# Optimization experiments

Measured on AMD Instinct MI355X. Metric: run time of the kernel, lower is better.

The kernel has to match this reference:

```python
import jax, jax.numpy as jnp
import numpy as np
from math import factorial, sqrt

# ---------------- irreps / instruction metadata ----------------
LS = [0, 1, 2]
MULS_IN = [128, 64, 32]      # node_irreps = 128x0e + 64x1o + 32x2e
HC = 32                      # hidden_channels -> mixed_irreps = 32x0e+32x1o+32x2e
# feasible 'uuw' instructions (parity-even outputs 0e,1e,2e)
INSTR = [(0,0,0),(1,1,0),(2,2,0),(1,1,1),(2,2,1),(0,2,2),(2,0,2),(1,1,2),(2,2,2)]
PATHS = {0: 3, 1: 2, 2: 4}

# ---------------- real Clebsch-Gordan coefficients ----------------
def _cg(l1, l2, l3):
    """Complex CG <l1 m1 l2 m2 | l3 m3>, shape [2l1+1,2l2+1,2l3+1]."""
    f = lambda n: float(factorial(n))
    C = np.zeros((2*l1+1, 2*l2+1, 2*l3+1))
    for m1 in range(-l1, l1+1):
        for m2 in range(-l2, l2+1):
            m3 = m1 + m2
            if abs(m3) > l3:
                continue
            pre = sqrt((2*l3+1) * f(l1+l2-l3)*f(l1-l2+l3)*f(-l1+l2+l3)/f(l1+l2+l3+1))
            pre *= sqrt(f(l3+m3)*f(l3-m3)*f(l1-m1)*f(l1+m1)*f(l2-m2)*f(l2+m2))
            s = 0.0
            for k in range(0, l1+l2-l3+1):
                d = [k, l1+l2-l3-k, l1-m1-k, l2+m2-k, l3-l2+m1+k, l3-l1-m2+k]
                if any(x < 0 for x in d):
                    continue
                s += (-1)**k / np.prod([f(x) for x in d])
            C[m1+l1, m2+l2, m3+l3] = pre * s
    return C

def _u_real(l):
    """Complex->real spherical harmonic change of basis (rows: real m)."""
    U = np.zeros((2*l+1, 2*l+1), dtype=complex)
    U[l, l] = 1.0
    for m in range(1, l+1):
        U[l+m, l+m] = (-1)**m / sqrt(2)
        U[l+m, l-m] = 1.0 / sqrt(2)
        U[l-m, l+m] = -1j*(-1)**m / sqrt(2)
        U[l-m, l-m] = 1j / sqrt(2)
    return U

def _real_cg(l1, l2, l3):
    """Real CG tensor, Frobenius norm 1 (like e3nn wigner_3j)."""
    C = _cg(l1, l2, l3).astype(complex)
    R = np.einsum('am,bn,co,mno->abc', _u_real(l1), _u_real(l2), np.conj(_u_real(l3)), C)
    Rr = R.real if np.abs(R.real).max() >= np.abs(R.imag).max() else R.imag
    return (Rr / np.linalg.norm(Rr)).astype(np.float32)

RCG = {k: _real_cg(*k) for k in set(INSTR)}
# Cartesian rank-2 change of basis: 3x3 tensor = 0e + 1e + 2e; orthonormal basis matrices
QB = {l: _real_cg(1, 1, l) * sqrt(2*l + 1) for l in LS}   # [3,3,2l+1]

def _split(x, muls):
    outs, off = [], 0
    for mul, l in zip(muls, LS):
        d = mul * (2*l + 1)
        outs.append(x[:, off:off+d].reshape(-1, mul, 2*l + 1))
        off += d
    return outs


def setup_inputs() -> dict:
    key = jax.random.key(0)
    ks = jax.random.split(key, 14)
    N, B = 50000, 500
    dim_sph = sum(m*(2*l+1) for m, l in zip(MULS_IN, LS))   # 480
    return {
        'x_scalar':    jax.random.normal(ks[0], (N, 128), jnp.float32),
        'x_spherical': jax.random.normal(ks[1], (N, dim_sph), jnp.float32),
        'batch':       jnp.sort(jax.random.randint(ks[2], (N,), 0, B)),
        'num_graphs':  B,
        'W0': jax.random.normal(ks[3], (128, HC), jnp.float32),
        'W1': jax.random.normal(ks[4], (64,  HC), jnp.float32),
        'W2': jax.random.normal(ks[5], (32,  HC), jnp.float32),
        'A1': jax.random.normal(ks[6], (128, 64), jnp.float32) / sqrt(128),
        'b1': jnp.zeros((64,), jnp.float32),
        'A2': jax.random.normal(ks[7], (64, 9*HC), jnp.float32) / sqrt(64),
        'b2': jnp.zeros((9*HC,), jnp.float32),
        'p0': jax.random.normal(ks[8], (3,), jnp.float32),
        'p1': jax.random.normal(ks[9], (2,), jnp.float32),
        'p2': jax.random.normal(ks[10], (4,), jnp.float32),
    }


def reference(x_scalar, x_spherical, batch, num_graphs,
              W0, W1, W2, A1, b1, A2, b2, p0, p1, p2):
    # ---- SelfMixTP: per-l linear mix to HC channels + per-irrep-block RMS norm ----
    xs_in = _split(x_spherical, MULS_IN)
    xs = []
    for x, W in zip(xs_in, [W0, W1, W2]):
        y = jnp.einsum('num,uv->nvm', x, W) / sqrt(W.shape[0])
        rms = jnp.sqrt(jnp.mean(y*y, axis=(1, 2), keepdims=True) + 1e-5)
        xs.append(y / rms)                       # [N, HC, 2l+1]
    # ---- per-node TP weights ----
    h = jax.nn.silu(x_scalar @ A1 + b1)
    tp_w = h @ A2 + b2                           # [N, 9*HC]
    # ---- weighted uuw CG tensor product ----
    outs = {0: [], 1: [], 2: []}
    off = 0
    for (la, lb, lo) in INSTR:
        w = tp_w[:, off:off+HC]; off += HC       # [N, HC]
        R = jnp.asarray(RCG[(la, lb, lo)])       # [2la+1, 2lb+1, 2lo+1]
        alpha = sqrt(2*lo + 1.0) / sqrt(PATHS[lo] * HC)
        xa = xs[la] * w[:, :, None]              # fold per-node weights into one factor
        y = jnp.einsum('nua,abc->nubc', xa, R)
        y = jnp.einsum('nubc,nub->nc', y, xs[lb]) * alpha
        outs[lo].append(y)
    # ---- post linear: collapse paths per l (sph_irreps -> rtp_irreps) ----
    sph = []
    for l, p in zip(LS, [p0, p1, p2]):
        stk = jnp.stack(outs[l], axis=1)         # [N, P_l, 2l+1]
        sph.append(jnp.einsum('npm,p->nm', stk, p) / sqrt(stk.shape[1]))
    # ---- Sph2Cart: spherical (0e+1e+2e) -> cartesian 3x3 ----
    x_cart = sum(jnp.einsum('nm,ijm->nij', sph[l], jnp.asarray(QB[l])) for l in LS)
    # ---- scatter-sum over graphs ----
    g = jax.ops.segment_sum(x_cart, batch, num_segments=num_graphs)  # [B,3,3]
    # ---- roll each cartesian axis by 1 (yzx -> xyz reordering) ----
    return jnp.roll(jnp.roll(g, 1, axis=1), 1, axis=2)
```

## Files before the change

### kernel.cpp

```cpp
#include <hip/hip_runtime.h>
#include <math.h>


#define N_CG_FLOATS 438

typedef short s16x8 __attribute__((ext_vector_type(8)));
typedef short s16x4 __attribute__((ext_vector_type(4)));
typedef float f32x4 __attribute__((ext_vector_type(4)));

#define PK_BYTE_OFF 2048
#define PK_A1 0
#define PK_W0 8192
#define PK_A2 12288
#define PK_W1 30720
#define PK_W2 32768
#define PK_TOTAL 33792

__device__ __forceinline__ short f2bf(float f) {
  union { float f; unsigned u; } x; x.f = f;
  unsigned r = (x.u + 0x7FFFu + ((x.u >> 16) & 1u)) >> 16;
  return (short)r;
}
__device__ __forceinline__ float bf2f(unsigned short s) {
  union { unsigned u; float f; } x; x.u = ((unsigned)s) << 16;
  return x.f;
}


__device__ __forceinline__ double dfact(int n) {
  double r = 1.0;
  for (int i = 2; i <= n; ++i) r *= (double)i;
  return r;
}

__device__ __forceinline__ void u_elem(int l, int i, int j, double& re, double& im) {
  re = 0.0; im = 0.0;
  const int mr = i - l, mc = j - l;
  const double is2 = 0.70710678118654752440;
  if (mr == 0) { if (mc == 0) re = 1.0; }
  else if (mr > 0) {
    if (mc == mr) re = ((mr & 1) ? -1.0 : 1.0) * is2;
    else if (mc == -mr) re = is2;
  } else {
    int m = -mr;
    if (mc == m) im = -(((m & 1) ? -1.0 : 1.0)) * is2;
    else if (mc == -m) im = is2;
  }
}

__global__ void setup_cg_par(float* __restrict__ ws) {
  const int LAs[12] = {0, 1, 2, 1, 2, 0, 2, 1, 2, 1, 1, 1};
  const int LBs[12] = {0, 1, 2, 1, 2, 2, 0, 1, 2, 1, 1, 1};
  const int LOs[12] = {0, 0, 0, 1, 1, 2, 2, 2, 2, 0, 1, 2};
  const int OFF[12] = {0, 1, 10, 35, 62, 137, 162, 187, 232, 357, 366, 393};

  const int blk = blockIdx.x;
  const int l1 = LAs[blk], l2 = LBs[blk], l3 = LOs[blk];
  const double scale = (blk >= 9) ? sqrt(2.0 * l3 + 1.0) : 1.0;
  const int n1 = 2 * l1 + 1, n2 = 2 * l2 + 1, n3 = 2 * l3 + 1;
  const int nel = n1 * n2 * n3;
  const int t = threadIdx.x;

  __shared__ double Cs[125];
  __shared__ double Rre[125], Rim[125];
  __shared__ double s_inv;
  __shared__ int s_useRe;

  if (t < nel) {
    const int i3 = t % n3, i2 = (t / n3) % n2, i1 = t / (n3 * n2);
    const int m1 = i1 - l1, m2 = i2 - l2, m3 = i3 - l3;
    double val = 0.0;
    if (m1 + m2 == m3) {
      double pre = sqrt((2.0 * l3 + 1.0) * dfact(l1 + l2 - l3) * dfact(l1 - l2 + l3) *
                        dfact(-l1 + l2 + l3) / dfact(l1 + l2 + l3 + 1));
      pre *= sqrt(dfact(l3 + m3) * dfact(l3 - m3) * dfact(l1 - m1) * dfact(l1 + m1) *
                  dfact(l2 - m2) * dfact(l2 + m2));
      double s = 0.0;
      for (int k = 0; k <= l1 + l2 - l3; ++k) {
        int d1 = l1 + l2 - l3 - k, d2 = l1 - m1 - k, d3 = l2 + m2 - k;
        int d4 = l3 - l2 + m1 + k, d5 = l3 - l1 - m2 + k;
        if (d1 < 0 || d2 < 0 || d3 < 0 || d4 < 0 || d5 < 0) continue;
        double prod = dfact(k) * dfact(d1) * dfact(d2) * dfact(d3) * dfact(d4) * dfact(d5);
        s += ((k & 1) ? -1.0 : 1.0) / prod;
      }
      val = pre * s;
    }
    Cs[t] = val;
  }
  __syncthreads();

  if (t < nel) {
    const int c = t % n3, bb = (t / n3) % n2, a = t / (n3 * n2);
    double sr_ = 0.0, si_ = 0.0;
    for (int m = 0; m < n1; ++m) {
      double u1r, u1i;
      u_elem(l1, a, m, u1r, u1i);
      if (u1r == 0.0 && u1i == 0.0) continue;
      for (int nn = 0; nn < n2; ++nn) {
        double u2r, u2i;
        u_elem(l2, bb, nn, u2r, u2i);
        double t12r = u1r * u2r - u1i * u2i;
        double t12i = u1r * u2i + u1i * u2r;
        if (t12r == 0.0 && t12i == 0.0) continue;
        for (int o = 0; o < n3; ++o) {
          double cgv = Cs[(m * n2 + nn) * n3 + o];
          if (cgv == 0.0) continue;
          double u3r, u3i;
          u_elem(l3, c, o, u3r, u3i);
          sr_ += (t12r * u3r + t12i * u3i) * cgv;
          si_ += (t12i * u3r - t12r * u3i) * cgv;
        }
      }
    }
    Rre[t] = sr_;
    Rim[t] = si_;
  }
  __syncthreads();

  if (t == 0) {
    double maxRe = 0.0, maxIm = 0.0;
    for (int e = 0; e < nel; ++e) {
      maxRe = fmax(maxRe, fabs(Rre[e]));
      maxIm = fmax(maxIm, fabs(Rim[e]));
    }
    int useRe = (maxRe >= maxIm) ? 1 : 0;
    double nrm = 0.0;
    for (int e = 0; e < nel; ++e) {
      double vv = useRe ? Rre[e] : Rim[e];
      nrm += vv * vv;
    }
    s_useRe = useRe;
    s_inv = scale / sqrt(nrm);
  }
  __syncthreads();

  if (t < nel) {
    double vv = s_useRe ? Rre[t] : Rim[t];
    ws[OFF[blk] + t] = (float)(vv * s_inv);
  }
}

__global__ void pack_weights(const float* __restrict__ A1, const float* __restrict__ W0,
                             const float* __restrict__ A2, const float* __restrict__ W1,
                             const float* __restrict__ W2, float* __restrict__ ws) {
  unsigned short* pk = (unsigned short*)((char*)ws + PK_BYTE_OFF);
  int e = blockIdx.x * 256 + threadIdx.x;
  if (e >= PK_TOTAL) return;
  const float* src;
  int Ncols, off;
  float scale;
  if (e < PK_W0)      { src = A1; Ncols = 64;  off = PK_A1; scale = 1.f; }
  else if (e < PK_A2) { src = W0; Ncols = 32;  off = PK_W0; scale = 0.08838834764831845f; }
  else if (e < PK_W1) { src = A2; Ncols = 288; off = PK_A2; scale = 1.f; }
  else if (e < PK_W2) { src = W1; Ncols = 32;  off = PK_W1; scale = 0.125f; }
  else                { src = W2; Ncols = 32;  off = PK_W2; scale = 0.17677669529663687f; }
  int local = e - off;
  int frag = local >> 9;
  int l = (local >> 3) & 63;
  int j = local & 7;
  int ntn = Ncols >> 4;
  int kt = frag / ntn, nt = frag - kt * ntn;
  int k = kt * 32 + 8 * (l >> 4) + j;
  int c = nt * 16 + (l & 15);
  pk[e] = (unsigned short)f2bf(src[k * Ncols + c] * scale);
}


__device__ __forceinline__ s16x8 cvt8(const float* __restrict__ g) {
  float4 a = *(const float4*)g;
  float4 b = *(const float4*)(g + 4);
  s16x8 r;
  r[0] = f2bf(a.x); r[1] = f2bf(a.y); r[2] = f2bf(a.z); r[3] = f2bf(a.w);
  r[4] = f2bf(b.x); r[5] = f2bf(b.y); r[6] = f2bf(b.z); r[7] = f2bf(b.w);
  return r;
}

__device__ __forceinline__ void sw_wr8(char* sm, int base, int strideB, int r, int c0, s16x8 v) {
  int byte = base + r * strideB + c0 * 2;
  byte ^= (r & 7) << 4;
  *(s16x8*)(sm + byte) = v;
}
__device__ __forceinline__ s16x8 sw_lda16(const char* sm, int base, int strideB, int k0,
                                          int lane) {
  int r = lane & 15;
  int byte = base + r * strideB + (k0 + 8 * (lane >> 4)) * 2;
  byte ^= (r & 7) << 4;
  return *(const s16x8*)(sm + byte);
}

template <int LA, int LB, int LO>
__device__ __forceinline__ void tp_accum(const float* __restrict__ R, float w,
                                         const float* xa, const float* xb, float* sph) {
  constexpr int NA = 2 * LA + 1, NB = 2 * LB + 1, NC = 2 * LO + 1;
#pragma unroll
  for (int a = 0; a < NA; ++a) {
#pragma unroll
    for (int b = 0; b < NB; ++b) {
      float xab = xa[a] * xb[b] * w;
#pragma unroll
      for (int c = 0; c < NC; ++c) sph[c] = fmaf(xab, R[(a * NB + b) * NC + c], sph[c]);
    }
  }
}

#define F_XS 0
#define F_SP 4096
#define F_H  8192
#define F_P1 10240
#define F_P2 16384
#define F_TW 10240
#define F_YA 21504
#define F_SMEM 30720

__global__ __launch_bounds__(256) void mega_fused(
    const float* __restrict__ xs_g, const float* __restrict__ sp_g,
    const int* __restrict__ batch, const float* __restrict__ b1,
    const float* __restrict__ b2, const float* __restrict__ p0,
    const float* __restrict__ p1, const float* __restrict__ p2,
    const float* __restrict__ ws, float* __restrict__ out, int N) {
  __shared__ char sm[F_SMEM];
  const unsigned short* pk = (const unsigned short*)((const char*)ws + PK_BYTE_OFF);
  const float* cg = ws;

  const int t = threadIdx.x;
  const int b0 = blockIdx.x * 16;
  const int lane = t & 63;
  const int wid = t >> 6;

  {
    int n = t >> 4, c0 = (t & 15) * 8;
    long nn = min((long)(b0 + n), (long)N - 1);
    sw_wr8(sm, F_XS, 256, n, c0, cvt8(xs_g + nn * 128 + c0));
    sw_wr8(sm, F_SP, 256, n, c0, cvt8(sp_g + nn * 480 + c0));
  }
  {
    int n = t >> 4, uc = t & 15;
    long nn = min((long)(b0 + n), (long)N - 1);
    const float* g = sp_g + nn * 480 + 128 + uc * 12;
    float4 a0 = *(const float4*)(g), a1 = *(const float4*)(g + 4), a2 = *(const float4*)(g + 8);
    float fl[12] = {a0.x, a0.y, a0.z, a0.w, a1.x, a1.y, a1.z, a1.w, a2.x, a2.y, a2.z, a2.w};
#pragma unroll
    for (int m = 0; m < 3; ++m) {
      s16x4 e;
#pragma unroll
      for (int j = 0; j < 4; ++j) e[j] = f2bf(fl[j * 3 + m]);
      int byte = F_P1 + m * 2048 + n * 128 + uc * 8;
      byte ^= (n & 7) << 4;
      *(s16x4*)(sm + byte) = e;
    }
  }
  if (t < 128) {
    int n = t >> 3, uc = t & 7;
    long nn = min((long)(b0 + n), (long)N - 1);
    const float* g = sp_g + nn * 480 + 320 + uc * 20;
    float4 a0 = *(const float4*)(g), a1 = *(const float4*)(g + 4), a2 = *(const float4*)(g + 8),
           a3 = *(const float4*)(g + 12), a4 = *(const float4*)(g + 16);
    float fl[20] = {a0.x, a0.y, a0.z, a0.w, a1.x, a1.y, a1.z, a1.w, a2.x, a2.y,
                    a2.z, a2.w, a3.x, a3.y, a3.z, a3.w, a4.x, a4.y, a4.z, a4.w};
#pragma unroll
    for (int m = 0; m < 5; ++m) {
      s16x4 e;
#pragma unroll
      for (int j = 0; j < 4; ++j) e[j] = f2bf(fl[j * 5 + m]);
      int byte = F_P2 + m * 1024 + n * 64 + uc * 8;
      byte ^= (n & 7) << 4;
      *(s16x4*)(sm + byte) = e;
    }
  }
  __syncthreads();

  {
    f32x4 acc = {0.f, 0.f, 0.f, 0.f};
#pragma unroll
    for (int kt = 0; kt < 4; ++kt) {
      s16x8 a = sw_lda16(sm, F_XS, 256, kt * 32, lane);
      s16x8 b = *(const s16x8*)(pk + PK_A1 + (((kt << 2) + wid) * 64 + lane) * 8);
      acc = __builtin_amdgcn_mfma_f32_16x16x32_bf16(a, b, acc, 0, 0, 0);
    }
    const int col = wid * 16 + (lane & 15);
    const int r0 = (lane >> 4) * 4;
    const float bb = b1[col];
#pragma unroll
    for (int q = 0; q < 4; ++q) {
      float hv = acc[q] + bb;
      hv = hv / (1.f + __expf(-hv));
      int r = r0 + q;
      int byte = F_H + r * 128 + col * 2;
      byte ^= (r & 7) << 4;
      *(short*)(sm + byte) = f2bf(hv);
    }
  }

  const int r0 = (lane >> 4) * 4;
  if (wid < 2) {
    f32x4 acc = {0.f, 0.f, 0.f, 0.f};
#pragma unroll
    for (int kt = 0; kt < 4; ++kt) {
      s16x8 a = sw_lda16(sm, F_SP, 256, kt * 32, lane);
      s16x8 b = *(const s16x8*)(pk + PK_W0 + (((kt << 1) + wid) * 64 + lane) * 8);
      acc = __builtin_amdgcn_mfma_f32_16x16x32_bf16(a, b, acc, 0, 0, 0);
    }
    const int col = wid * 16 + (lane & 15);
#pragma unroll
    for (int q = 0; q < 4; ++q)
      *(short*)(sm + F_YA + (r0 + q) * 576 + col * 2) = f2bf(acc[q]);
  }
  for (int tl = wid; tl < 6; tl += 4) {
    const int m = tl >> 1, nt = tl & 1;
    f32x4 acc = {0.f, 0.f, 0.f, 0.f};
#pragma unroll
    for (int kt = 0; kt < 2; ++kt) {
      s16x8 a = sw_lda16(sm, F_P1 + m * 2048, 128, kt * 32, lane);
      s16x8 b = *(const s16x8*)(pk + PK_W1 + (((kt << 1) + nt) * 64 + lane) * 8);
      acc = __builtin_amdgcn_mfma_f32_16x16x32_bf16(a, b, acc, 0, 0, 0);
    }
    const int col = 32 + m * 32 + nt * 16 + (lane & 15);
#pragma unroll
    for (int q = 0; q < 4; ++q)
      *(short*)(sm + F_YA + (r0 + q) * 576 + col * 2) = f2bf(acc[q]);
  }
  for (int tl = wid; tl < 10; tl += 4) {
    const int m = tl >> 1, nt = tl & 1;
    f32x4 acc = {0.f, 0.f, 0.f, 0.f};
    {
      s16x8 a = sw_lda16(sm, F_P2 + m * 1024, 64, 0, lane);
      s16x8 b = *(const s16x8*)(pk + PK_W2 + (nt * 64 + lane) * 8);
      acc = __builtin_amdgcn_mfma_f32_16x16x32_bf16(a, b, acc, 0, 0, 0);
    }
    const int col = 128 + m * 32 + nt * 16 + (lane & 15);
#pragma unroll
    for (int q = 0; q < 4; ++q)
      *(short*)(sm + F_YA + (r0 + q) * 576 + col * 2) = f2bf(acc[q]);
  }
  __syncthreads();

  for (int tl = wid; tl < 18; tl += 4) {
    f32x4 acc = {0.f, 0.f, 0.f, 0.f};
#pragma unroll
    for (int kt = 0; kt < 2; ++kt) {
      s16x8 a = sw_lda16(sm, F_H, 128, kt * 32, lane);
      s16x8 b = *(const s16x8*)(pk + PK_A2 + ((kt * 18 + tl) * 64 + lane) * 8);
      acc = __builtin_amdgcn_mfma_f32_16x16x32_bf16(a, b, acc, 0, 0, 0);
    }
    const int col = tl * 16 + (lane & 15);
    const float bb = b2[col];
#pragma unroll
    for (int q = 0; q < 4; ++q)
      *(short*)(sm + F_TW + (r0 + q) * 576 + col * 2) = f2bf(acc[q] + bb);
  }
  __syncthreads();

  const int v = t & 31;
  const int sl = t >> 5;
  const float invs32 = 0.17677669529663687f;
  const float k0c = invs32 / 3.0f;
  const float k1c = 1.7320508075688772f * invs32 / 2.0f;
  const float k2c = 2.23606797749979f * invs32 / 4.0f;
  const float c0 = k0c * p0[0], c1 = k0c * p0[1], c2 = k0c * p0[2];
  const float c3 = k1c * p1[0], c4 = k1c * p1[1];
  const float c5 = k2c * p2[0], c6 = k2c * p2[1], c7 = k2c * p2[2], c8 = k2c * p2[3];
  const float* qb0 = cg + 357;
  const float* qb1 = cg + 366;
  const float* qb2 = cg + 393;

#pragma unroll 1
  for (int r = 0; r < 2; ++r) {
    const int nrow = sl + 8 * r;
    const int n = b0 + nrow;
    const unsigned short* yb = (const unsigned short*)(sm + F_YA + nrow * 576);
    const unsigned short* tb = (const unsigned short*)(sm + F_TW + nrow * 576);

    const float y0v = bf2f(yb[v]);
    float y1[3], y2[5];
#pragma unroll
    for (int m = 0; m < 3; ++m) y1[m] = bf2f(yb[32 + m * 32 + v]);
#pragma unroll
    for (int m = 0; m < 5; ++m) y2[m] = bf2f(yb[128 + m * 32 + v]);

    float s0 = y0v * y0v;
    float s1 = y1[0] * y1[0] + y1[1] * y1[1] + y1[2] * y1[2];
    float s2 = 0.f;
#pragma unroll
    for (int m = 0; m < 5; ++m) s2 = fmaf(y2[m], y2[m], s2);
#pragma unroll
    for (int msk = 16; msk >= 1; msk >>= 1) {
      s0 += __shfl_xor(s0, msk);
      s1 += __shfl_xor(s1, msk);
      s2 += __shfl_xor(s2, msk);
    }
    const float i0 = 1.0f / sqrtf(s0 * (1.0f / 32.0f) + 1e-5f);
    const float i1 = 1.0f / sqrtf(s1 * (1.0f / 96.0f) + 1e-5f);
    const float i2 = 1.0f / sqrtf(s2 * (1.0f / 160.0f) + 1e-5f);
    float xs0[1] = {y0v * i0};
    float xs1[3], xs2[5];
#pragma unroll
    for (int m = 0; m < 3; ++m) xs1[m] = y1[m] * i1;
#pragma unroll
    for (int m = 0; m < 5; ++m) xs2[m] = y2[m] * i2;

    float w9[9];
#pragma unroll
    for (int i = 0; i < 9; ++i) w9[i] = bf2f(tb[i * 32 + v]);

    float sph0[1] = {0.f};
    float sph1[3] = {0.f, 0.f, 0.f};
    float sph2[5] = {0.f, 0.f, 0.f, 0.f, 0.f};
    tp_accum<0, 0, 0>(cg + 0,   w9[0] * c0, xs0, xs0, sph0);
    tp_accum<1, 1, 0>(cg + 1,   w9[1] * c1, xs1, xs1, sph0);
    tp_accum<2, 2, 0>(cg + 10,  w9[2] * c2, xs2, xs2, sph0);
    tp_accum<1, 1, 1>(cg + 35,  w9[3] * c3, xs1, xs1, sph1);
    tp_accum<2, 2, 1>(cg + 62,  w9[4] * c4, xs2, xs2, sph1);
    tp_accum<0, 2, 2>(cg + 137, w9[5] * c5, xs0, xs2, sph2);
    tp_accum<2, 0, 2>(cg + 162, w9[6] * c6, xs2, xs0, sph2);
    tp_accum<1, 1, 2>(cg + 187, w9[7] * c7, xs1, xs1, sph2);
    tp_accum<2, 2, 2>(cg + 232, w9[8] * c8, xs2, xs2, sph2);

#pragma unroll
    for (int msk = 16; msk >= 1; msk >>= 1) {
      sph0[0] += __shfl_xor(sph0[0], msk);
#pragma unroll
      for (int m = 0; m < 3; ++m) sph1[m] += __shfl_xor(sph1[m], msk);
#pragma unroll
      for (int m = 0; m < 5; ++m) sph2[m] += __shfl_xor(sph2[m], msk);
    }

    if (v < 9 && n < N) {
      const int i = v / 3, j = v - 3 * i;
      float val = sph0[0] * qb0[v];
#pragma unroll
      for (int m = 0; m < 3; ++m) val = fmaf(sph1[m], qb1[v * 3 + m], val);
#pragma unroll
      for (int m = 0; m < 5; ++m) val = fmaf(sph2[m], qb2[v * 5 + m], val);
      float* og = out + (long)batch[n] * 9;
      atomicAdd(&og[((i + 1) % 3) * 3 + ((j + 1) % 3)], val);
    }
  }
}


extern "C" void kernel_launch(void* const* d_in, const int* in_sizes, int n_in,
                              void* d_out, int out_size, void* d_ws, size_t ws_size,
                              hipStream_t stream) {
  const float* x_scalar = (const float*)d_in[0];
  const float* x_sph    = (const float*)d_in[1];
  const int*   batch    = (const int*)d_in[2];
  const float* W0 = (const float*)d_in[4];
  const float* W1 = (const float*)d_in[5];
  const float* W2 = (const float*)d_in[6];
  const float* A1 = (const float*)d_in[7];
  const float* b1 = (const float*)d_in[8];
  const float* A2 = (const float*)d_in[9];
  const float* b2 = (const float*)d_in[10];
  const float* p0 = (const float*)d_in[11];
  const float* p1 = (const float*)d_in[12];
  const float* p2 = (const float*)d_in[13];
  float* out = (float*)d_out;
  float* ws  = (float*)d_ws;

  const int N = in_sizes[0] / 128;

  hipMemsetAsync(d_out, 0, (size_t)out_size * sizeof(float), stream);
  setup_cg_par<<<12, 128, 0, stream>>>(ws);
  pack_weights<<<(PK_TOTAL + 255) / 256, 256, 0, stream>>>(A1, W0, A2, W1, W2, ws);
  const int blocks = (N + 15) / 16;
  mega_fused<<<blocks, 256, 0, stream>>>(x_scalar, x_sph, batch, b1, b2, p0, p1, p2,
                                         ws, out, N);
}
```

Baseline: 121.0 us.

## Double block threads to 512 and redistribute load, GEMM and TP work

The fused kernel now launches 512 threads (8 waves) per 16-node block instead of 256. Input staging is split between the two halves. The first MLP GEMM and the W0 projection run concurrently on separate waves, and the other GEMM tiles are strided over 8 waves. Each 32-lane group handles one node in the tensor-product stage instead of looping over two. This adds parallelism per block and shortens serial per-thread work, at the cost of larger blocks and possibly lower occupancy per CU.

```diff
diff --git a/kernel.cpp b/kernel.cpp
--- a/kernel.cpp
+++ b/kernel.cpp
@@ -212,7 +212,7 @@
 #define F_YA 21504
 #define F_SMEM 30720
 
-__global__ __launch_bounds__(256) void mega_fused(
+__global__ __launch_bounds__(512) void mega_fused(
     const float* __restrict__ xs_g, const float* __restrict__ sp_g,
     const int* __restrict__ batch, const float* __restrict__ b1,
     const float* __restrict__ b2, const float* __restrict__ p0,
@@ -227,16 +227,11 @@
   const int lane = t & 63;
   const int wid = t >> 6;
 
-  {
+  if (t < 256) {
     int n = t >> 4, c0 = (t & 15) * 8;
     long nn = min((long)(b0 + n), (long)N - 1);
     sw_wr8(sm, F_XS, 256, n, c0, cvt8(xs_g + nn * 128 + c0));
-    sw_wr8(sm, F_SP, 256, n, c0, cvt8(sp_g + nn * 480 + c0));
-  }
-  {
-    int n = t >> 4, uc = t & 15;
-    long nn = min((long)(b0 + n), (long)N - 1);
-    const float* g = sp_g + nn * 480 + 128 + uc * 12;
+    const float* g = sp_g + nn * 480 + 128 + (t & 15) * 12;
     float4 a0 = *(const float4*)(g), a1 = *(const float4*)(g + 4), a2 = *(const float4*)(g + 8);
     float fl[12] = {a0.x, a0.y, a0.z, a0.w, a1.x, a1.y, a1.z, a1.w, a2.x, a2.y, a2.z, a2.w};
 #pragma unroll
@@ -244,32 +239,38 @@
       s16x4 e;
 #pragma unroll
       for (int j = 0; j < 4; ++j) e[j] = f2bf(fl[j * 3 + m]);
-      int byte = F_P1 + m * 2048 + n * 128 + uc * 8;
+      int byte = F_P1 + m * 2048 + n * 128 + (t & 15) * 8;
       byte ^= (n & 7) << 4;
       *(s16x4*)(sm + byte) = e;
     }
-  }
-  if (t < 128) {
-    int n = t >> 3, uc = t & 7;
+  } else {
+    int u = t - 256;
+    int n = u >> 4, c0 = (u & 15) * 8;
     long nn = min((long)(b0 + n), (long)N - 1);
-    const float* g = sp_g + nn * 480 + 320 + uc * 20;
-    float4 a0 = *(const float4*)(g), a1 = *(const float4*)(g + 4), a2 = *(const float4*)(g + 8),
-           a3 = *(const float4*)(g + 12), a4 = *(const float4*)(g + 16);
-    float fl[20] = {a0.x, a0.y, a0.z, a0.w, a1.x, a1.y, a1.z, a1.w, a2.x, a2.y,
-                    a2.z, a2.w, a3.x, a3.y, a3.z, a3.w, a4.x, a4.y, a4.z, a4.w};
-#pragma unroll
-    for (int m = 0; m < 5; ++m) {
-      s16x4 e;
-#pragma unroll
-      for (int j = 0; j < 4; ++j) e[j] = f2bf(fl[j * 5 + m]);
-      int byte = F_P2 + m * 1024 + n * 64 + uc * 8;
-      byte ^= (n & 7) << 4;
-      *(s16x4*)(sm + byte) = e;
-    }
-  }
-  __syncthreads();
-
-  {
+    sw_wr8(sm, F_SP, 256, n, c0, cvt8(sp_g + nn * 480 + c0));
+    if (u < 128) {
+      int n2_ = u >> 3, uc = u & 7;
+      long nn2 = min((long)(b0 + n2_), (long)N - 1);
+      const float* g = sp_g + nn2 * 480 + 320 + uc * 20;
+      float4 a0 = *(const float4*)(g), a1 = *(const float4*)(g + 4), a2 = *(const float4*)(g + 8),
+             a3 = *(const float4*)(g + 12), a4 = *(const float4*)(g + 16);
+      float fl[20] = {a0.x, a0.y, a0.z, a0.w, a1.x, a1.y, a1.z, a1.w, a2.x, a2.y,
+                      a2.z, a2.w, a3.x, a3.y, a3.z, a3.w, a4.x, a4.y, a4.z, a4.w};
+#pragma unroll
+      for (int m = 0; m < 5; ++m) {
+        s16x4 e;
+#pragma unroll
+        for (int j = 0; j < 4; ++j) e[j] = f2bf(fl[j * 5 + m]);
+        int byte = F_P2 + m * 1024 + n2_ * 64 + uc * 8;
+        byte ^= (n2_ & 7) << 4;
+        *(s16x4*)(sm + byte) = e;
+      }
+    }
+  }
+  __syncthreads();
+
+  const int r0 = (lane >> 4) * 4;
+  if (wid < 4) {
     f32x4 acc = {0.f, 0.f, 0.f, 0.f};
 #pragma unroll
     for (int kt = 0; kt < 4; ++kt) {
@@ -278,7 +279,6 @@
       acc = __builtin_amdgcn_mfma_f32_16x16x32_bf16(a, b, acc, 0, 0, 0);
     }
     const int col = wid * 16 + (lane & 15);
-    const int r0 = (lane >> 4) * 4;
     const float bb = b1[col];
 #pragma unroll
     for (int q = 0; q < 4; ++q) {
@@ -289,23 +289,21 @@
       byte ^= (r & 7) << 4;
       *(short*)(sm + byte) = f2bf(hv);
     }
-  }
-
-  const int r0 = (lane >> 4) * 4;
-  if (wid < 2) {
+  } else if (wid < 6) {
+    const int nt = wid - 4;
     f32x4 acc = {0.f, 0.f, 0.f, 0.f};
 #pragma unroll
     for (int kt = 0; kt < 4; ++kt) {
       s16x8 a = sw_lda16(sm, F_SP, 256, kt * 32, lane);
-      s16x8 b = *(const s16x8*)(pk + PK_W0 + (((kt << 1) + wid) * 64 + lane) * 8);
+      s16x8 b = *(const s16x8*)(pk + PK_W0 + (((kt << 1) + nt) * 64 + lane) * 8);
       acc = __builtin_amdgcn_mfma_f32_16x16x32_bf16(a, b, acc, 0, 0, 0);
     }
-    const int col = wid * 16 + (lane & 15);
+    const int col = nt * 16 + (lane & 15);
 #pragma unroll
     for (int q = 0; q < 4; ++q)
       *(short*)(sm + F_YA + (r0 + q) * 576 + col * 2) = f2bf(acc[q]);
   }
-  for (int tl = wid; tl < 6; tl += 4) {
+  for (int tl = wid; tl < 6; tl += 8) {
     const int m = tl >> 1, nt = tl & 1;
     f32x4 acc = {0.f, 0.f, 0.f, 0.f};
 #pragma unroll
@@ -319,7 +317,7 @@
     for (int q = 0; q < 4; ++q)
       *(short*)(sm + F_YA + (r0 + q) * 576 + col * 2) = f2bf(acc[q]);
   }
-  for (int tl = wid; tl < 10; tl += 4) {
+  for (int tl = wid; tl < 10; tl += 8) {
     const int m = tl >> 1, nt = tl & 1;
     f32x4 acc = {0.f, 0.f, 0.f, 0.f};
     {
@@ -334,7 +332,7 @@
   }
   __syncthreads();
 
-  for (int tl = wid; tl < 18; tl += 4) {
+  for (int tl = wid; tl < 18; tl += 8) {
     f32x4 acc = {0.f, 0.f, 0.f, 0.f};
 #pragma unroll
     for (int kt = 0; kt < 2; ++kt) {
@@ -363,77 +361,73 @@
   const float* qb1 = cg + 366;
   const float* qb2 = cg + 393;
 
-#pragma unroll 1
-  for (int r = 0; r < 2; ++r) {
-    const int nrow = sl + 8 * r;
-    const int n = b0 + nrow;
-    const unsigned short* yb = (const unsigned short*)(sm + F_YA + nrow * 576);
-    const unsigned short* tb = (const unsigned short*)(sm + F_TW + nrow * 576);
-
-    const float y0v = bf2f(yb[v]);
-    float y1[3], y2[5];
-#pragma unroll
-    for (int m = 0; m < 3; ++m) y1[m] = bf2f(yb[32 + m * 32 + v]);
-#pragma unroll
-    for (int m = 0; m < 5; ++m) y2[m] = bf2f(yb[128 + m * 32 + v]);
-
-    float s0 = y0v * y0v;
-    float s1 = y1[0] * y1[0] + y1[1] * y1[1] + y1[2] * y1[2];
-    float s2 = 0.f;
-#pragma unroll
-    for (int m = 0; m < 5; ++m) s2 = fmaf(y2[m], y2[m], s2);
-#pragma unroll
-    for (int msk = 16; msk >= 1; msk >>= 1) {
-      s0 += __shfl_xor(s0, msk);
-      s1 += __shfl_xor(s1, msk);
-      s2 += __shfl_xor(s2, msk);
-    }
-    const float i0 = 1.0f / sqrtf(s0 * (1.0f / 32.0f) + 1e-5f);
-    const float i1 = 1.0f / sqrtf(s1 * (1.0f / 96.0f) + 1e-5f);
-    const float i2 = 1.0f / sqrtf(s2 * (1.0f / 160.0f) + 1e-5f);
-    float xs0[1] = {y0v * i0};
-    float xs1[3], xs2[5];
-#pragma unroll
-    for (int m = 0; m < 3; ++m) xs1[m] = y1[m] * i1;
-#pragma unroll
-    for (int m = 0; m < 5; ++m) xs2[m] = y2[m] * i2;
-
-    float w9[9];
-#pragma unroll
-    for (int i = 0; i < 9; ++i) w9[i] = bf2f(tb[i * 32 + v]);
-
-    float sph0[1] = {0.f};
-    float sph1[3] = {0.f, 0.f, 0.f};
-    float sph2[5] = {0.f, 0.f, 0.f, 0.f, 0.f};
-    tp_accum<0, 0, 0>(cg + 0,   w9[0] * c0, xs0, xs0, sph0);
-    tp_accum<1, 1, 0>(cg + 1,   w9[1] * c1, xs1, xs1, sph0);
-    tp_accum<2, 2, 0>(cg + 10,  w9[2] * c2, xs2, xs2, sph0);
-    tp_accum<1, 1, 1>(cg + 35,  w9[3] * c3, xs1, xs1, sph1);
-    tp_accum<2, 2, 1>(cg + 62,  w9[4] * c4, xs2, xs2, sph1);
-    tp_accum<0, 2, 2>(cg + 137, w9[5] * c5, xs0, xs2, sph2);
-    tp_accum<2, 0, 2>(cg + 162, w9[6] * c6, xs2, xs0, sph2);
-    tp_accum<1, 1, 2>(cg + 187, w9[7] * c7, xs1, xs1, sph2);
-    tp_accum<2, 2, 2>(cg + 232, w9[8] * c8, xs2, xs2, sph2);
-
-#pragma unroll
-    for (int msk = 16; msk >= 1; msk >>= 1) {
-      sph0[0] += __shfl_xor(sph0[0], msk);
-#pragma unroll
-      for (int m = 0; m < 3; ++m) sph1[m] += __shfl_xor(sph1[m], msk);
-#pragma unroll
-      for (int m = 0; m < 5; ++m) sph2[m] += __shfl_xor(sph2[m], msk);
-    }
-
-    if (v < 9 && n < N) {
-      const int i = v / 3, j = v - 3 * i;
-      float val = sph0[0] * qb0[v];
-#pragma unroll
-      for (int m = 0; m < 3; ++m) val = fmaf(sph1[m], qb1[v * 3 + m], val);
-#pragma unroll
-      for (int m = 0; m < 5; ++m) val = fmaf(sph2[m], qb2[v * 5 + m], val);
-      float* og = out + (long)batch[n] * 9;
-      atomicAdd(&og[((i + 1) % 3) * 3 + ((j + 1) % 3)], val);
-    }
+  const int n = b0 + sl;
+  const unsigned short* yb = (const unsigned short*)(sm + F_YA + sl * 576);
+  const unsigned short* tb = (const unsigned short*)(sm + F_TW + sl * 576);
+
+  const float y0v = bf2f(yb[v]);
+  float y1[3], y2[5];
+#pragma unroll
+  for (int m = 0; m < 3; ++m) y1[m] = bf2f(yb[32 + m * 32 + v]);
+#pragma unroll
+  for (int m = 0; m < 5; ++m) y2[m] = bf2f(yb[128 + m * 32 + v]);
+
+  float s0 = y0v * y0v;
+  float s1 = y1[0] * y1[0] + y1[1] * y1[1] + y1[2] * y1[2];
+  float s2 = 0.f;
+#pragma unroll
+  for (int m = 0; m < 5; ++m) s2 = fmaf(y2[m], y2[m], s2);
+#pragma unroll
+  for (int msk = 16; msk >= 1; msk >>= 1) {
+    s0 += __shfl_xor(s0, msk);
+    s1 += __shfl_xor(s1, msk);
+    s2 += __shfl_xor(s2, msk);
+  }
+  const float i0 = 1.0f / sqrtf(s0 * (1.0f / 32.0f) + 1e-5f);
+  const float i1 = 1.0f / sqrtf(s1 * (1.0f / 96.0f) + 1e-5f);
+  const float i2 = 1.0f / sqrtf(s2 * (1.0f / 160.0f) + 1e-5f);
+  float xs0[1] = {y0v * i0};
+  float xs1[3], xs2[5];
+#pragma unroll
+  for (int m = 0; m < 3; ++m) xs1[m] = y1[m] * i1;
+#pragma unroll
+  for (int m = 0; m < 5; ++m) xs2[m] = y2[m] * i2;
+
+  float w9[9];
+#pragma unroll
+  for (int i = 0; i < 9; ++i) w9[i] = bf2f(tb[i * 32 + v]);
+
+  float sph0[1] = {0.f};
+  float sph1[3] = {0.f, 0.f, 0.f};
+  float sph2[5] = {0.f, 0.f, 0.f, 0.f, 0.f};
+  tp_accum<0, 0, 0>(cg + 0,   w9[0] * c0, xs0, xs0, sph0);
+  tp_accum<1, 1, 0>(cg + 1,   w9[1] * c1, xs1, xs1, sph0);
+  tp_accum<2, 2, 0>(cg + 10,  w9[2] * c2, xs2, xs2, sph0);
+  tp_accum<1, 1, 1>(cg + 35,  w9[3] * c3, xs1, xs1, sph1);
+  tp_accum<2, 2, 1>(cg + 62,  w9[4] * c4, xs2, xs2, sph1);
+  tp_accum<0, 2, 2>(cg + 137, w9[5] * c5, xs0, xs2, sph2);
+  tp_accum<2, 0, 2>(cg + 162, w9[6] * c6, xs2, xs0, sph2);
+  tp_accum<1, 1, 2>(cg + 187, w9[7] * c7, xs1, xs1, sph2);
+  tp_accum<2, 2, 2>(cg + 232, w9[8] * c8, xs2, xs2, sph2);
+
+#pragma unroll
+  for (int msk = 16; msk >= 1; msk >>= 1) {
+    sph0[0] += __shfl_xor(sph0[0], msk);
+#pragma unroll
+    for (int m = 0; m < 3; ++m) sph1[m] += __shfl_xor(sph1[m], msk);
+#pragma unroll
+    for (int m = 0; m < 5; ++m) sph2[m] += __shfl_xor(sph2[m], msk);
+  }
+
+  if (v < 9 && n < N) {
+    const int i = v / 3, j = v - 3 * i;
+    float val = sph0[0] * qb0[v];
+#pragma unroll
+    for (int m = 0; m < 3; ++m) val = fmaf(sph1[m], qb1[v * 3 + m], val);
+#pragma unroll
+    for (int m = 0; m < 5; ++m) val = fmaf(sph2[m], qb2[v * 5 + m], val);
+    float* og = out + (long)batch[n] * 9;
+    atomicAdd(&og[((i + 1) % 3) * 3 + ((j + 1) % 3)], val);
   }
 }
 
@@ -463,6 +457,6 @@
   setup_cg_par<<<12, 128, 0, stream>>>(ws);
   pack_weights<<<(PK_TOTAL + 255) / 256, 256, 0, stream>>>(A1, W0, A2, W1, W2, ws);
   const int blocks = (N + 15) / 16;
-  mega_fused<<<blocks, 256, 0, stream>>>(x_scalar, x_sph, batch, b1, b2, p0, p1, p2,
+  mega_fused<<<blocks, 512, 0, stream>>>(x_scalar, x_sph, batch, b1, b2, p0, p1, p2,
                                          ws, out, N);
 }
```

After: 107.9 us (median of 2 runs). 1.12x faster.
